# Kernel tuning notes

Measured on AMD Instinct MI355X. Metric: run time of the kernel, lower is better.

## Reference

```python
import jax, jax.numpy as jnp
import numpy as np

NUM_PRICAPS, DIM_PRICAPS = 1152, 8
NUM_OBJCAPS, DIM_OBJCAPS = 10, 16
ROUTINGS = 3


def squash(v, axis=-1):
    norm = jnp.linalg.norm(v, axis=axis, keepdims=True)
    scale = norm ** 2 / (1.0 + norm ** 2) / (norm + 1e-8)
    return scale * v


def conv2d(x, w, b, stride):
    out = jax.lax.conv_general_dilated(
        x, w, window_strides=(stride, stride), padding='VALID',
        dimension_numbers=('NCHW', 'OIHW', 'NCHW'))
    return out + b[None, :, None, None]


def setup_inputs() -> dict:
    key = jax.random.key(0)
    ks = jax.random.split(key, 12)
    f32 = jnp.float32
    x = jax.random.uniform(ks[0], (512, 1, 28, 28), dtype=f32)
    conv1_w = jax.random.normal(ks[1], (256, 1, 9, 9), f32) / np.sqrt(1 * 81)
    conv1_b = jnp.zeros((256,), f32)
    conv2_w = jax.random.normal(ks[2], (256, 256, 9, 9), f32) / np.sqrt(256 * 81)
    conv2_b = jnp.zeros((256,), f32)
    route_w = 0.1 * jax.random.normal(ks[3], (NUM_OBJCAPS, NUM_PRICAPS, DIM_OBJCAPS, DIM_PRICAPS), f32)
    d_in = NUM_OBJCAPS * DIM_OBJCAPS  # 160
    dec1_w = jax.random.normal(ks[4], (512, d_in), f32) / np.sqrt(d_in)
    dec1_b = jnp.zeros((512,), f32)
    dec2_w = jax.random.normal(ks[5], (1024, 512), f32) / np.sqrt(512)
    dec2_b = jnp.zeros((1024,), f32)
    dec3_w = jax.random.normal(ks[6], (784, 1024), f32) / np.sqrt(1024)
    dec3_b = jnp.zeros((784,), f32)
    return {'x': x, 'conv1_w': conv1_w, 'conv1_b': conv1_b,
            'conv2_w': conv2_w, 'conv2_b': conv2_b, 'route_w': route_w,
            'dec1_w': dec1_w, 'dec1_b': dec1_b, 'dec2_w': dec2_w,
            'dec2_b': dec2_b, 'dec3_w': dec3_w, 'dec3_b': dec3_b}


def reference(x, conv1_w, conv1_b, conv2_w, conv2_b, route_w,
              dec1_w, dec1_b, dec2_w, dec2_b, dec3_w, dec3_b):
    B = x.shape[0]
    # Encoder: two convs (no activation in original), then capsulate + squash
    h = conv2d(x, conv1_w, conv1_b, 1)            # [B,256,20,20]
    h = conv2d(h, conv2_w, conv2_b, 2)            # [B,256,6,6]
    pricaps = squash(jnp.transpose(h, (0, 2, 3, 1)).reshape(B, NUM_PRICAPS, DIM_PRICAPS))
    # Votes: weight [o,i,k,d] @ incaps [b,i,d] -> [b,o,i,k]
    hat = jnp.einsum('oikd,bid->boik', route_w, pricaps)  # [B,10,1152,16]
    hat_det = jax.lax.stop_gradient(hat)
    b_log = jnp.zeros((B, NUM_OBJCAPS, NUM_PRICAPS), x.dtype)
    c = jax.nn.softmax(jnp.ones((B, NUM_OBJCAPS, NUM_PRICAPS), x.dtype), axis=1)
    outcaps = None
    for i in range(ROUTINGS):
        if i < ROUTINGS - 1:
            outcaps = squash(jnp.sum(c[:, :, :, None] * hat_det, axis=2, keepdims=True))  # [B,10,1,16]
            b_log = b_log + jnp.sum(outcaps * hat_det, axis=-1)
            c = jax.nn.softmax(b_log, axis=1)
        else:
            outcaps = squash(jnp.sum(c[:, :, :, None] * hat, axis=2, keepdims=True))
    objcaps = outcaps[:, :, 0, :]                 # [B,10,16]
    objcaps_len = jnp.linalg.norm(objcaps, axis=-1)  # [B,10]
    # Decoder: reconstruct only the max-length class capsule
    idx_max = jnp.argmax(objcaps_len, axis=1)
    y_onehot = jax.nn.one_hot(idx_max, NUM_OBJCAPS, dtype=objcaps.dtype)
    oc = (objcaps * y_onehot[:, :, None]).reshape(B, -1)  # [B,160]
    d = jax.nn.relu(oc @ dec1_w.T + dec1_b)
    d = jax.nn.relu(d @ dec2_w.T + dec2_b)
    d = jax.nn.sigmoid(d @ dec3_w.T + dec3_b)
    x_recon = jnp.clip(d.reshape(B, 1, 28, 28), 0.0, 1.0)
    return (objcaps_len, x_recon)
```

## Files before the change

### kernel.cpp

```cpp
#include <hip/hip_runtime.h>

typedef short short8 __attribute__((ext_vector_type(8)));
typedef float floatx4 __attribute__((ext_vector_type(4)));

__device__ __forceinline__ unsigned short bf16rn(float x) {
  union { float f; unsigned int u; } v; v.f = x;
  unsigned int r = v.u + 0x7fffu + ((v.u >> 16) & 1u);
  return (unsigned short)(r >> 16);
}
__device__ __forceinline__ float bf16f(unsigned short h) {
  union { unsigned int u; float f; } v; v.u = ((unsigned int)h) << 16;
  return v.f;
}
__device__ __forceinline__ void gload16(const void* g, void* l) {
  __builtin_amdgcn_global_load_lds((const __attribute__((address_space(1))) unsigned int*)g,
                                   (__attribute__((address_space(3))) unsigned int*)l, 16, 0, 0);
}
__device__ __forceinline__ unsigned swz128(int row) {
  return ((row & 1) << 6) | ((row & 2) << 4) | ((row & 4) << 2);
}
__device__ __forceinline__ unsigned s4of(int row) {
  return ((row & 1) << 2) | (row & 2) | ((row & 4) >> 2);
}

__global__ __launch_bounds__(256) void k_w2p(const float* __restrict__ w2,
                                             unsigned short* __restrict__ w2p) {
  __shared__ float sm[20736];
  const int t = threadIdx.x;
  const int co = blockIdx.x;
  for (int q = t; q < 20736; q += 256) sm[q] = w2[(size_t)co * 20736 + q];
  __syncthreads();
  const unsigned s4 = s4of(co);
  unsigned short* base = w2p + (size_t)co * 64;
  for (int q = t; q < 5184; q += 256) {
    int kk = q >> 6, r = q & 63, cb = r >> 3, cp = r & 7;
    unsigned src = (unsigned)cp ^ s4;
    int half = src >> 2, oct = src & 3;
    const float* col = &sm[(cb * 32 + oct * 8) * 81 + kk];
    union { unsigned short u[8]; uint4 v; } pk;
#pragma unroll
    for (int j = 0; j < 8; ++j) {
      float v = col[j * 81];
      unsigned short hi = bf16rn(v);
      pk.u[j] = half ? bf16rn(v - bf16f(hi)) : hi;
    }
    *(uint4*)(base + (size_t)(kk * 8 + cb) * 16384 + cp * 8) = pk.v;
  }
}

__global__ __launch_bounds__(256) void k_conv1(const float* __restrict__ x, const float* __restrict__ w1,
                                               const float* __restrict__ b1,
                                               unsigned short* __restrict__ h1h,
                                               unsigned short* __restrict__ h1l, int b0) {
  __shared__ float xs[784];
  __shared__ float wsm[64 * 81];
  const int t = threadIdx.x;
  const int b = b0 + blockIdx.x;
  const int coq = blockIdx.y;
  for (int q = t; q < 784; q += 256) xs[q] = x[(size_t)b * 784 + q];
  for (int q = t; q < 5184; q += 256) wsm[q] = w1[coq * 5184 + q];
  __syncthreads();
  const int col = t & 63, yg = t >> 6;
  const int co = coq * 64 + col;
  const float bv = b1[co];
  unsigned short* oh = h1h + (size_t)blockIdx.x * 102400 + co;
  unsigned short* ol = h1l + (size_t)blockIdx.x * 102400 + co;
  for (int yy = 0; yy < 5; ++yy) {
    const int y = yg * 5 + yy;
    float acc[20];
#pragma unroll
    for (int i = 0; i < 20; ++i) acc[i] = bv;
    for (int ky = 0; ky < 9; ++ky) {
      float row[28];
#pragma unroll
      for (int cc = 0; cc < 28; ++cc) row[cc] = xs[(y + ky) * 28 + cc];
#pragma unroll
      for (int kx = 0; kx < 9; ++kx) {
        float wv = wsm[col * 81 + ky * 9 + kx];
#pragma unroll
        for (int xx = 0; xx < 20; ++xx) acc[xx] += row[xx + kx] * wv;
      }
    }
#pragma unroll
    for (int xx = 0; xx < 20; ++xx) {
      unsigned short hi = bf16rn(acc[xx]);
      unsigned short lo = bf16rn(acc[xx] - bf16f(hi));
      size_t p = (size_t)(y * 20 + xx) * 256;
      oh[p] = hi; ol[p] = lo;
    }
  }
}

__global__ __launch_bounds__(256) void k_conv2m(const unsigned short* __restrict__ h1h,
                                                const unsigned short* __restrict__ h1l,
                                                const unsigned short* __restrict__ w2p,
                                                float* __restrict__ part, int b0) {
  __shared__ __align__(16) char smem[40960];
  const int t = threadIdx.x;
  const int lin = blockIdx.x + 144 * blockIdx.z;
  const int xcd = lin & 7, idx = lin >> 3;
  const int zz = xcd & 3;
  const int n0 = ((xcd >> 2) * 72 + idx) * 64;
  const int kk0 = (zz == 0) ? 0 : (21 + 20 * (zz - 1));
  const int kkn = (zz == 0) ? 21 : 20;

  const int wid = t >> 6, lane = t & 63;
  const int l15 = lane & 15, l4 = lane >> 4;
  const int brow = t >> 2, bc4 = t & 3;
  size_t bsrc;
  {
    int nloc = n0 + brow;
    int bi = nloc / 36, pp = nloc - bi * 36;
    int oy = pp / 6, ox = pp - oy * 6;
    bsrc = ((size_t)((bi * 20 + 2 * oy) * 20 + 2 * ox)) * 256;
  }
  const unsigned bswz = swz128(brow);
  const unsigned bo_hi = (unsigned)(brow * 128) + (((unsigned)(bc4 * 16)) ^ bswz);
  const unsigned bo_lo = (unsigned)(brow * 128) + (((unsigned)(64 + bc4 * 16)) ^ bswz);

  floatx4 acc[4][4];
#pragma unroll
  for (int i = 0; i < 4; ++i)
#pragma unroll
    for (int j = 0; j < 4; ++j) acc[i][j] = (floatx4)0.f;

  for (int kq = 0; kq < kkn; ++kq) {
    const int kk = kk0 + kq;
    const int ky = kk / 9, kx = kk - ky * 9;
    const int koff = (ky * 20 + kx) * 256;
    for (int cb = 0; cb < 8; ++cb) {
      const unsigned short* abase = w2p + (size_t)(kk * 8 + cb) * 16384;
#pragma unroll
      for (int j = 0; j < 8; ++j) {
        const int seg = j * 4 + wid;
        gload16(abase + seg * 512 + lane * 8, smem + seg * 1024);
      }
      {
        const unsigned short* sh = h1h + bsrc + koff + cb * 32 + bc4 * 8;
        const unsigned short* sl = h1l + bsrc + koff + cb * 32 + bc4 * 8;
        uint4 vh = *(const uint4*)sh;
        uint4 vl = *(const uint4*)sl;
        *(uint4*)(smem + 32768 + bo_hi) = vh;
        *(uint4*)(smem + 32768 + bo_lo) = vl;
      }
      __syncthreads();
      short8 bh[4], blo[4];
#pragma unroll
      for (int nf = 0; nf < 4; ++nf) {
        const int br = nf * 16 + l15;
        const unsigned s = swz128(br);
        bh[nf] = *(const short8*)(smem + 32768 + br * 128 + (((unsigned)(l4 * 16)) ^ s));
        blo[nf] = *(const short8*)(smem + 32768 + br * 128 + (((unsigned)(64 + l4 * 16)) ^ s));
      }
#pragma unroll
      for (int mf = 0; mf < 4; ++mf) {
        const int ar = wid * 64 + mf * 16 + l15;
        const unsigned s = swz128(ar);
        short8 ah = *(const short8*)(smem + ar * 128 + (((unsigned)(l4 * 16)) ^ s));
        short8 al = *(const short8*)(smem + ar * 128 + (((unsigned)(64 + l4 * 16)) ^ s));
#pragma unroll
        for (int nf = 0; nf < 4; ++nf) {
          acc[mf][nf] = __builtin_amdgcn_mfma_f32_16x16x32_bf16(ah, bh[nf], acc[mf][nf], 0, 0, 0);
          acc[mf][nf] = __builtin_amdgcn_mfma_f32_16x16x32_bf16(ah, blo[nf], acc[mf][nf], 0, 0, 0);
          acc[mf][nf] = __builtin_amdgcn_mfma_f32_16x16x32_bf16(al, bh[nf], acc[mf][nf], 0, 0, 0);
        }
      }
      __syncthreads();
    }
  }
  float* po = part + (size_t)zz * 4718592;
#pragma unroll
  for (int mf = 0; mf < 4; ++mf) {
#pragma unroll
    for (int nf = 0; nf < 4; ++nf) {
      int cog = wid * 64 + mf * 16 + l4 * 4;
      int ng = b0 * 36 + n0 + nf * 16 + l15;
      *(floatx4*)&po[(size_t)ng * 256 + cog] = acc[mf][nf];
    }
  }
}

__global__ __launch_bounds__(256) void k_redsquash(const float* __restrict__ part,
                                                   const float* __restrict__ b2,
                                                   float* __restrict__ pri) {
  const int idx = blockIdx.x * 256 + threadIdx.x;
  const int n = idx >> 5, cap = idx & 31;
  const size_t o = (size_t)n * 256 + cap * 8;
  float s[8];
#pragma unroll
  for (int j = 0; j < 8; ++j) s[j] = b2[cap * 8 + j];
#pragma unroll
  for (int z = 0; z < 4; ++z) {
    const float4 a0 = *(const float4*)&part[(size_t)z * 4718592 + o];
    const float4 a1 = *(const float4*)&part[(size_t)z * 4718592 + o + 4];
    s[0] += a0.x; s[1] += a0.y; s[2] += a0.z; s[3] += a0.w;
    s[4] += a1.x; s[5] += a1.y; s[6] += a1.z; s[7] += a1.w;
  }
  float ss = 0.f;
#pragma unroll
  for (int j = 0; j < 8; ++j) ss += s[j] * s[j];
  float nn = sqrtf(ss);
  float sc = ss / (1.f + ss) / (nn + 1e-8f);
  float4 o0, o1;
  o0.x = s[0] * sc; o0.y = s[1] * sc; o0.z = s[2] * sc; o0.w = s[3] * sc;
  o1.x = s[4] * sc; o1.y = s[5] * sc; o1.z = s[6] * sc; o1.w = s[7] * sc;
  *(float4*)&pri[o] = o0;
  *(float4*)&pri[o + 4] = o1;
}

__global__ __launch_bounds__(256) void k_rwp(const float* __restrict__ rw,
                                             unsigned short* __restrict__ rwpa) {
  __shared__ float sm[8192];
  const int t = threadIdx.x;
  const int o = blockIdx.x / 18, ic = blockIdx.x % 18;
  const float* src = rw + (size_t)o * 147456 + (size_t)ic * 8192;
  for (int q = t; q < 8192; q += 256) sm[q] = src[q];
  __syncthreads();
  const int r = t;
  const int c32 = r >> 4, kobj = r & 15;
  const unsigned s4 = s4of(r);
  unsigned short* base = rwpa + (size_t)blockIdx.x * 16384 + r * 64;
#pragma unroll
  for (int cp = 0; cp < 8; ++cp) {
    unsigned c = (unsigned)cp ^ s4;
    int half = c >> 2;
    int il = c32 * 4 + (c & 3);
    const float* col = &sm[il * 128 + kobj * 8];
    union { unsigned short u[8]; uint4 v; } pk;
#pragma unroll
    for (int e = 0; e < 8; ++e) {
      float v = col[e];
      unsigned short hi = bf16rn(v);
      pk.u[e] = half ? bf16rn(v - bf16f(hi)) : hi;
    }
    *(uint4*)(base + cp * 8) = pk.v;
  }
}

__global__ __launch_bounds__(256, 2) void k_passA(const unsigned short* __restrict__ rwpa,
                                                  const float* __restrict__ pri,
                                                  const float* __restrict__ cbuf,
                                                  float* __restrict__ spart, int iter) {
  __shared__ __align__(16) char smem[65536];
  const int t = threadIdx.x;
  const int b0 = blockIdx.x * 16, ic = blockIdx.y, o = blockIdx.z;
  const int i0 = ic * 64;
  {
    const unsigned short* abase = rwpa + (size_t)(o * 18 + ic) * 16384;
    const int wid = t >> 6, lane = t & 63;
#pragma unroll
    for (int j = 0; j < 8; ++j) {
      const int seg = j * 4 + wid;
      gload16(abase + seg * 512 + lane * 8, smem + seg * 1024);
    }
  }
  const int bl = t >> 4, c32 = t & 15;
  {
    const float* psrc = pri + (size_t)(b0 + bl) * 9216 + i0 * 8 + c32 * 32;
    float pv[32];
#pragma unroll
    for (int j = 0; j < 8; ++j) {
      float4 v = *(const float4*)&psrc[j * 4];
      pv[j * 4 + 0] = v.x; pv[j * 4 + 1] = v.y; pv[j * 4 + 2] = v.z; pv[j * 4 + 3] = v.w;
    }
    float cv[4];
    if (iter == 0) {
      cv[0] = cv[1] = cv[2] = cv[3] = 0.1f;
    } else {
      float4 cc = *(const float4*)&cbuf[(size_t)((b0 + bl) * 10 + o) * 1152 + i0 + c32 * 4];
      cv[0] = cc.x; cv[1] = cc.y; cv[2] = cc.z; cv[3] = cc.w;
    }
    union { unsigned short u[32]; uint4 v[4]; } qh, ql;
#pragma unroll
    for (int m = 0; m < 32; ++m) {
      float q = cv[m >> 3] * pv[m];
      unsigned short hi = bf16rn(q);
      qh.u[m] = hi;
      ql.u[m] = bf16rn(q - bf16f(hi));
    }
    const int r = c32 * 16 + bl;
    const unsigned swz = swz128(r);
    char* qbase = smem + 32768 + r * 128;
#pragma unroll
    for (int j = 0; j < 8; ++j) {
      int c = (j + c32) & 7;
      uint4 v = (c < 4) ? qh.v[c & 3] : ql.v[c & 3];
      *(uint4*)(qbase + (((unsigned)(c * 16)) ^ swz)) = v;
    }
  }
  __syncthreads();
  const int wid = t >> 6, lane = t & 63;
  const int l15 = lane & 15, l4 = lane >> 4;
  floatx4 acc = (floatx4)0.f;
#pragma unroll
  for (int cc = 0; cc < 4; ++cc) {
    const int kc = wid * 4 + cc;
    const int rr = kc * 16 + l15;
    const unsigned s = swz128(rr);
    short8 ah  = *(const short8*)(smem + rr * 128 + (((unsigned)(l4 * 16)) ^ s));
    short8 al  = *(const short8*)(smem + rr * 128 + (((unsigned)(64 + l4 * 16)) ^ s));
    short8 bh  = *(const short8*)(smem + 32768 + rr * 128 + (((unsigned)(l4 * 16)) ^ s));
    short8 blo = *(const short8*)(smem + 32768 + rr * 128 + (((unsigned)(64 + l4 * 16)) ^ s));
    acc = __builtin_amdgcn_mfma_f32_16x16x32_bf16(ah, bh, acc, 0, 0, 0);
    acc = __builtin_amdgcn_mfma_f32_16x16x32_bf16(ah, blo, acc, 0, 0, 0);
    acc = __builtin_amdgcn_mfma_f32_16x16x32_bf16(al, bh, acc, 0, 0, 0);
  }
  __syncthreads();
  *(floatx4*)(smem + wid * 1024 + (l15 * 16 + l4 * 4) * 4) = acc;
  __syncthreads();
  {
    const int obl = t >> 4, okj = t & 15;
    const float* pp = (const float*)smem;
    float s = pp[obl * 16 + okj] + pp[256 + obl * 16 + okj] +
              pp[512 + obl * 16 + okj] + pp[768 + obl * 16 + okj];
    spart[((size_t)blockIdx.y * 512 + (b0 + obl)) * 160 + o * 16 + okj] = s;
  }
}

__global__ __launch_bounds__(256) void k_reduce(const float* __restrict__ spart, float* __restrict__ outc,
                                                float* __restrict__ len_out, int final_) {
  const int t = threadIdx.x;
  const int b = blockIdx.x;
  if (t >= 160) return;
  const int o = t / 16, d = t & 15;
  float s = 0.f;
  for (int ic = 0; ic < 18; ++ic) s += spart[((size_t)ic * 512 + b) * 160 + t];
  float ss = s * s;
  ss += __shfl_xor(ss, 1, 16);
  ss += __shfl_xor(ss, 2, 16);
  ss += __shfl_xor(ss, 4, 16);
  ss += __shfl_xor(ss, 8, 16);
  float n = sqrtf(ss);
  float sc = ss / (1.f + ss) / (n + 1e-8f);
  outc[(size_t)b * 160 + t] = sc * s;
  if (final_ && d == 0) len_out[b * 10 + o] = sc * n;
}

__global__ __launch_bounds__(256, 2) void k_passB(const float* __restrict__ rw, const float* __restrict__ pri,
                                                  const float* __restrict__ outc, float* __restrict__ blog,
                                                  int accum) {
  __shared__ __align__(16) float rw_s[16 * 516];
  __shared__ __align__(16) float p_s[16 * 516];
  __shared__ float oc_s[256];
  const int t = threadIdx.x;
  const int b0 = blockIdx.x * 16, i0 = blockIdx.y * 64, o = blockIdx.z;
  const float* rsrc = rw + (size_t)o * 147456 + (size_t)i0 * 128;
  for (int m = t; m < 2048; m += 256) {
    int il = m >> 5, r = m & 31, d = r >> 1, kh = (m & 1) * 4;
    float4 v = *(const float4*)&rsrc[il * 128 + d * 8 + kh];
    *(float4*)&rw_s[d * 516 + il * 8 + kh] = v;
  }
  for (int m = t; m < 2048; m += 256) {
    int bl = m >> 7, off = (m & 127) * 4;
    float4 v = *(const float4*)&pri[(size_t)(b0 + bl) * 9216 + i0 * 8 + off];
    *(float4*)&p_s[bl * 516 + off] = v;
  }
  oc_s[t] = outc[(size_t)(b0 + (t >> 4)) * 160 + o * 16 + (t & 15)];
  __syncthreads();
  const int il0 = t & 15, bl = t >> 4;
  float ocv[16];
#pragma unroll
  for (int k = 0; k < 16; ++k) ocv[k] = oc_s[bl * 16 + k];
#pragma unroll
  for (int is = 0; is < 4; ++is) {
    const int il = is * 16 + il0;
    float4 p0 = *(float4*)&p_s[bl * 516 + il * 8];
    float4 p1 = *(float4*)&p_s[bl * 516 + il * 8 + 4];
    float acc = 0.f;
#pragma unroll
    for (int dd = 0; dd < 16; ++dd) {
      float4 r0 = *(float4*)&rw_s[dd * 516 + il * 8];
      float4 r1 = *(float4*)&rw_s[dd * 516 + il * 8 + 4];
      float h = r0.x * p0.x + r0.y * p0.y + r0.z * p0.z + r0.w * p0.w +
                r1.x * p1.x + r1.y * p1.y + r1.z * p1.z + r1.w * p1.w;
      acc += h * ocv[dd];
    }
    size_t gi = (size_t)((b0 + bl) * 10 + o) * 1152 + i0 + il;
    blog[gi] = accum ? (blog[gi] + acc) : acc;
  }
}

__global__ __launch_bounds__(256) void k_softmax(const float* __restrict__ blog, float* __restrict__ cbuf) {
  const int b = blockIdx.x;
  const int i = blockIdx.y * 256 + threadIdx.x;
  if (i >= 1152) return;
  float v[10];
  float m = -1e30f;
#pragma unroll
  for (int o = 0; o < 10; ++o) {
    v[o] = blog[(size_t)(b * 10 + o) * 1152 + i];
    m = fmaxf(m, v[o]);
  }
  float s = 0.f;
#pragma unroll
  for (int o = 0; o < 10; ++o) {
    v[o] = __expf(v[o] - m);
    s += v[o];
  }
  float inv = 1.f / s;
#pragma unroll
  for (int o = 0; o < 10; ++o) cbuf[(size_t)(b * 10 + o) * 1152 + i] = v[o] * inv;
}

__global__ __launch_bounds__(256) void k_argmax(const float* __restrict__ len_, const float* __restrict__ outc,
                                                int* __restrict__ win, float* __restrict__ oc16) {
  const int b = blockIdx.x * 256 + threadIdx.x;
  if (b >= 512) return;
  float best = len_[b * 10];
  int wi = 0;
  for (int o = 1; o < 10; ++o) {
    float v = len_[b * 10 + o];
    if (v > best) { best = v; wi = o; }
  }
  win[b] = wi;
  for (int k = 0; k < 16; ++k) oc16[b * 16 + k] = outc[(size_t)b * 160 + wi * 16 + k];
}

__global__ __launch_bounds__(256) void k_dec1(const float* __restrict__ oc16, const int* __restrict__ win,
                                              const float* __restrict__ w, const float* __restrict__ bias,
                                              float* __restrict__ d1) {
  const int b = blockIdx.x, t = threadIdx.x;
  const int wi = win[b];
  float ocv[16];
#pragma unroll
  for (int k = 0; k < 16; ++k) ocv[k] = oc16[b * 16 + k];
#pragma unroll
  for (int rep = 0; rep < 2; ++rep) {
    int j = t + rep * 256;
    const float* wr = w + (size_t)j * 160 + wi * 16;
    float acc = bias[j];
#pragma unroll
    for (int k = 0; k < 16; ++k) acc += ocv[k] * wr[k];
    d1[(size_t)b * 512 + j] = fmaxf(acc, 0.f);
  }
}

template <int K, int ACT>
__global__ __launch_bounds__(256) void k_fc(const float* __restrict__ in, const float* __restrict__ w,
                                            const float* __restrict__ bias, float* __restrict__ out, int M) {
  __shared__ __align__(16) float w_s[16 * 64];
  __shared__ __align__(16) float i_s[16 * 64];
  const int t = threadIdx.x;
  const int j0 = blockIdx.x * 64, b0 = blockIdx.y * 64;
  const int tx = t & 15, ty = t >> 4;
  const int jl = tx * 4, bl = ty * 4;
  float acc[4][4];
#pragma unroll
  for (int i = 0; i < 4; ++i)
#pragma unroll
    for (int j = 0; j < 4; ++j) acc[i][j] = 0.f;
  const int rr = t >> 2, kq = (t & 3) * 4;
  for (int k0 = 0; k0 < K; k0 += 16) {
    __syncthreads();
    float4 wv = make_float4(0.f, 0.f, 0.f, 0.f);
    if (j0 + rr < M) wv = *(const float4*)&w[(size_t)(j0 + rr) * K + k0 + kq];
    float4 iv = *(const float4*)&in[(size_t)(b0 + rr) * K + k0 + kq];
    w_s[(kq + 0) * 64 + rr] = wv.x;
    w_s[(kq + 1) * 64 + rr] = wv.y;
    w_s[(kq + 2) * 64 + rr] = wv.z;
    w_s[(kq + 3) * 64 + rr] = wv.w;
    i_s[(kq + 0) * 64 + rr] = iv.x;
    i_s[(kq + 1) * 64 + rr] = iv.y;
    i_s[(kq + 2) * 64 + rr] = iv.z;
    i_s[(kq + 3) * 64 + rr] = iv.w;
    __syncthreads();
#pragma unroll
    for (int k = 0; k < 16; ++k) {
      float4 a = *(float4*)&w_s[k * 64 + jl];
      float4 v = *(float4*)&i_s[k * 64 + bl];
      float av[4] = {a.x, a.y, a.z, a.w};
      float vv[4] = {v.x, v.y, v.z, v.w};
#pragma unroll
      for (int jj = 0; jj < 4; ++jj)
#pragma unroll
        for (int bb = 0; bb < 4; ++bb) acc[jj][bb] += av[jj] * vv[bb];
    }
  }
#pragma unroll
  for (int jj = 0; jj < 4; ++jj) {
    int j = j0 + jl + jj;
    if (j >= M) continue;
    float bs = bias[j];
#pragma unroll
    for (int bb = 0; bb < 4; ++bb) {
      float v = acc[jj][bb] + bs;
      if (ACT == 0) {
        v = fmaxf(v, 0.f);
      } else {
        v = 1.f / (1.f + __expf(-v));
        v = fminf(fmaxf(v, 0.f), 1.f);
      }
      out[(size_t)(b0 + bl + bb) * M + j] = v;
    }
  }
}

extern "C" void kernel_launch(void* const* d_in, const int* in_sizes, int n_in,
                              void* d_out, int out_size, void* d_ws, size_t ws_size,
                              hipStream_t stream) {
  (void)in_sizes; (void)n_in; (void)out_size; (void)ws_size;
  const float* x   = (const float*)d_in[0];
  const float* w1  = (const float*)d_in[1];
  const float* b1  = (const float*)d_in[2];
  const float* w2  = (const float*)d_in[3];
  const float* b2  = (const float*)d_in[4];
  const float* rw  = (const float*)d_in[5];
  const float* d1w = (const float*)d_in[6];
  const float* d1b = (const float*)d_in[7];
  const float* d2w = (const float*)d_in[8];
  const float* d2b = (const float*)d_in[9];
  const float* d3w = (const float*)d_in[10];
  const float* d3b = (const float*)d_in[11];
  float* out = (float*)d_out;

  char* wsb = (char*)d_ws;
  size_t cur = 0;
  auto alloc = [&](size_t bytes) -> char* {
    char* p = wsb + cur;
    cur += (bytes + 255) & ~(size_t)255;
    return p;
  };
  unsigned short* W2P = (unsigned short*)alloc(21233664);
  float* PART = (float*)alloc(75497472);
  float* PRI  = (float*)alloc(18874368);
  float* OUTC = (float*)alloc(327680);
  float* OC   = (float*)alloc(32768);
  int*   WIN  = (int*)alloc(2048);
  float* D1   = (float*)alloc(1048576);
  float* D2   = (float*)alloc(2097152);
  unsigned short* H1H = (unsigned short*)alloc(52428800);
  unsigned short* H1L = (unsigned short*)alloc(52428800);
  float* C  = (float*)H1H;
  float* BL = (float*)((char*)H1H + 23592960);
  float* SP = (float*)((char*)H1H + 47185920);
  unsigned short* RWPA = (unsigned short*)PART;

  k_w2p<<<256, 256, 0, stream>>>(w2, W2P);
  for (int b0 = 0; b0 < 512; b0 += 256) {
    k_conv1<<<dim3(256, 4), 256, 0, stream>>>(x, w1, b1, H1H, H1L, b0);
    k_conv2m<<<dim3(144, 1, 4), 256, 0, stream>>>(H1H, H1L, W2P, PART, b0);
  }
  k_redsquash<<<2304, 256, 0, stream>>>(PART, b2, PRI);
  k_rwp<<<180, 256, 0, stream>>>(rw, RWPA);

  dim3 gAB(32, 18, 10);
  k_passA<<<gAB, 256, 0, stream>>>(RWPA, PRI, C, SP, 0);
  k_reduce<<<512, 256, 0, stream>>>(SP, OUTC, out, 0);
  k_passB<<<gAB, 256, 0, stream>>>(rw, PRI, OUTC, BL, 0);
  k_softmax<<<dim3(512, 5), 256, 0, stream>>>(BL, C);
  k_passA<<<gAB, 256, 0, stream>>>(RWPA, PRI, C, SP, 1);
  k_reduce<<<512, 256, 0, stream>>>(SP, OUTC, out, 0);
  k_passB<<<gAB, 256, 0, stream>>>(rw, PRI, OUTC, BL, 1);
  k_softmax<<<dim3(512, 5), 256, 0, stream>>>(BL, C);
  k_passA<<<gAB, 256, 0, stream>>>(RWPA, PRI, C, SP, 2);
  k_reduce<<<512, 256, 0, stream>>>(SP, OUTC, out, 1);

  k_argmax<<<2, 256, 0, stream>>>(out, OUTC, WIN, OC);
  k_dec1<<<512, 256, 0, stream>>>(OC, WIN, d1w, d1b, D1);
  k_fc<512, 0><<<dim3(16, 8), 256, 0, stream>>>(D1, d2w, d2b, D2, 1024);
  k_fc<1024, 1><<<dim3(13, 8), 256, 0, stream>>>(D2, d3w, d3b, out + 5120, 784);
}
```

Measured before the change: 1.414 ms.

## Fuse routing pass A with squash reduce by looping over input-capsule chunks

The routing vote-sum kernel now loops over all 18 input-capsule chunks inside one block, accumulating in MFMA registers, then applies squash and writes output capsules directly. This removes the separate partial-sum buffer and the reduce kernel launch. The grid shrinks from 5760 blocks to 320 and each block runs the chunks serially with full syncs and no load/compute overlap, which may reduce parallelism and latency hiding on the GPU. The k_rwp indexing was simplified to an equivalent linear offset.

```diff
diff --git a/kernel.cpp b/kernel.cpp
--- a/kernel.cpp
+++ b/kernel.cpp
@@ -212,8 +212,7 @@
                                              unsigned short* __restrict__ rwpa) {
   __shared__ float sm[8192];
   const int t = threadIdx.x;
-  const int o = blockIdx.x / 18, ic = blockIdx.x % 18;
-  const float* src = rw + (size_t)o * 147456 + (size_t)ic * 8192;
+  const float* src = rw + (size_t)blockIdx.x * 8192;
   for (int q = t; q < 8192; q += 256) sm[q] = src[q];
   __syncthreads();
   const int r = t;
@@ -237,94 +236,84 @@
   }
 }
 
-__global__ __launch_bounds__(256, 2) void k_passA(const unsigned short* __restrict__ rwpa,
-                                                  const float* __restrict__ pri,
-                                                  const float* __restrict__ cbuf,
-                                                  float* __restrict__ spart, int iter) {
+__global__ __launch_bounds__(256, 2) void k_passAf(const unsigned short* __restrict__ rwpa,
+                                                   const float* __restrict__ pri,
+                                                   const float* __restrict__ cbuf,
+                                                   float* __restrict__ outc,
+                                                   float* __restrict__ len_out,
+                                                   int iter, int final_) {
   __shared__ __align__(16) char smem[65536];
   const int t = threadIdx.x;
-  const int b0 = blockIdx.x * 16, ic = blockIdx.y, o = blockIdx.z;
-  const int i0 = ic * 64;
-  {
-    const unsigned short* abase = rwpa + (size_t)(o * 18 + ic) * 16384;
-    const int wid = t >> 6, lane = t & 63;
-#pragma unroll
-    for (int j = 0; j < 8; ++j) {
-      const int seg = j * 4 + wid;
-      gload16(abase + seg * 512 + lane * 8, smem + seg * 1024);
-    }
-  }
-  const int bl = t >> 4, c32 = t & 15;
-  {
-    const float* psrc = pri + (size_t)(b0 + bl) * 9216 + i0 * 8 + c32 * 32;
-    float pv[32];
-#pragma unroll
-    for (int j = 0; j < 8; ++j) {
-      float4 v = *(const float4*)&psrc[j * 4];
-      pv[j * 4 + 0] = v.x; pv[j * 4 + 1] = v.y; pv[j * 4 + 2] = v.z; pv[j * 4 + 3] = v.w;
-    }
-    float cv[4];
-    if (iter == 0) {
-      cv[0] = cv[1] = cv[2] = cv[3] = 0.1f;
-    } else {
-      float4 cc = *(const float4*)&cbuf[(size_t)((b0 + bl) * 10 + o) * 1152 + i0 + c32 * 4];
-      cv[0] = cc.x; cv[1] = cc.y; cv[2] = cc.z; cv[3] = cc.w;
-    }
-    union { unsigned short u[32]; uint4 v[4]; } qh, ql;
-#pragma unroll
-    for (int m = 0; m < 32; ++m) {
-      float q = cv[m >> 3] * pv[m];
-      unsigned short hi = bf16rn(q);
-      qh.u[m] = hi;
-      ql.u[m] = bf16rn(q - bf16f(hi));
-    }
-    const int r = c32 * 16 + bl;
-    const unsigned swz = swz128(r);
-    char* qbase = smem + 32768 + r * 128;
-#pragma unroll
-    for (int j = 0; j < 8; ++j) {
-      int c = (j + c32) & 7;
-      uint4 v = (c < 4) ? qh.v[c & 3] : ql.v[c & 3];
-      *(uint4*)(qbase + (((unsigned)(c * 16)) ^ swz)) = v;
-    }
-  }
-  __syncthreads();
+  const int b0 = blockIdx.x * 16, o = blockIdx.y;
   const int wid = t >> 6, lane = t & 63;
   const int l15 = lane & 15, l4 = lane >> 4;
+  const int bl = t >> 4, c32 = t & 15;
+
   floatx4 acc = (floatx4)0.f;
-#pragma unroll
-  for (int cc = 0; cc < 4; ++cc) {
-    const int kc = wid * 4 + cc;
-    const int rr = kc * 16 + l15;
-    const unsigned s = swz128(rr);
-    short8 ah  = *(const short8*)(smem + rr * 128 + (((unsigned)(l4 * 16)) ^ s));
-    short8 al  = *(const short8*)(smem + rr * 128 + (((unsigned)(64 + l4 * 16)) ^ s));
-    short8 bh  = *(const short8*)(smem + 32768 + rr * 128 + (((unsigned)(l4 * 16)) ^ s));
-    short8 blo = *(const short8*)(smem + 32768 + rr * 128 + (((unsigned)(64 + l4 * 16)) ^ s));
-    acc = __builtin_amdgcn_mfma_f32_16x16x32_bf16(ah, bh, acc, 0, 0, 0);
-    acc = __builtin_amdgcn_mfma_f32_16x16x32_bf16(ah, blo, acc, 0, 0, 0);
-    acc = __builtin_amdgcn_mfma_f32_16x16x32_bf16(al, bh, acc, 0, 0, 0);
-  }
-  __syncthreads();
+  for (int ic = 0; ic < 18; ++ic) {
+    const int i0 = ic * 64;
+    {
+      const unsigned short* abase = rwpa + (size_t)(o * 18 + ic) * 16384;
+#pragma unroll
+      for (int j = 0; j < 8; ++j) {
+        const int seg = j * 4 + wid;
+        gload16(abase + seg * 512 + lane * 8, smem + seg * 1024);
+      }
+    }
+    {
+      const float* psrc = pri + (size_t)(b0 + bl) * 9216 + i0 * 8 + c32 * 32;
+      float pv[32];
+#pragma unroll
+      for (int j = 0; j < 8; ++j) {
+        float4 v = *(const float4*)&psrc[j * 4];
+        pv[j * 4 + 0] = v.x; pv[j * 4 + 1] = v.y; pv[j * 4 + 2] = v.z; pv[j * 4 + 3] = v.w;
+      }
+      float cv[4];
+      if (iter == 0) {
+        cv[0] = cv[1] = cv[2] = cv[3] = 0.1f;
+      } else {
+        float4 cc = *(const float4*)&cbuf[(size_t)((b0 + bl) * 10 + o) * 1152 + i0 + c32 * 4];
+        cv[0] = cc.x; cv[1] = cc.y; cv[2] = cc.z; cv[3] = cc.w;
+      }
+      union { unsigned short u[32]; uint4 v[4]; } qh, ql;
+#pragma unroll
+      for (int m = 0; m < 32; ++m) {
+        float q = cv[m >> 3] * pv[m];
+        unsigned short hi = bf16rn(q);
+        qh.u[m] = hi;
+        ql.u[m] = bf16rn(q - bf16f(hi));
+      }
+      const int r = c32 * 16 + bl;
+      const unsigned swz = swz128(r);
+      char* qbase = smem + 32768 + r * 128;
+#pragma unroll
+      for (int j = 0; j < 8; ++j) {
+        int c = (j + c32) & 7;
+        uint4 v = (c < 4) ? qh.v[c & 3] : ql.v[c & 3];
+        *(uint4*)(qbase + (((unsigned)(c * 16)) ^ swz)) = v;
+      }
+    }
+    __syncthreads();
+#pragma unroll
+    for (int cc = 0; cc < 4; ++cc) {
+      const int kc = wid * 4 + cc;
+      const int rr = kc * 16 + l15;
+      const unsigned s = swz128(rr);
+      short8 ah  = *(const short8*)(smem + rr * 128 + (((unsigned)(l4 * 16)) ^ s));
+      short8 al  = *(const short8*)(smem + rr * 128 + (((unsigned)(64 + l4 * 16)) ^ s));
+      short8 bh  = *(const short8*)(smem + 32768 + rr * 128 + (((unsigned)(l4 * 16)) ^ s));
+      short8 blo = *(const short8*)(smem + 32768 + rr * 128 + (((unsigned)(64 + l4 * 16)) ^ s));
+      acc = __builtin_amdgcn_mfma_f32_16x16x32_bf16(ah, bh, acc, 0, 0, 0);
+      acc = __builtin_amdgcn_mfma_f32_16x16x32_bf16(ah, blo, acc, 0, 0, 0);
+      acc = __builtin_amdgcn_mfma_f32_16x16x32_bf16(al, bh, acc, 0, 0, 0);
+    }
+    __syncthreads();
+  }
   *(floatx4*)(smem + wid * 1024 + (l15 * 16 + l4 * 4) * 4) = acc;
   __syncthreads();
-  {
-    const int obl = t >> 4, okj = t & 15;
-    const float* pp = (const float*)smem;
-    float s = pp[obl * 16 + okj] + pp[256 + obl * 16 + okj] +
-              pp[512 + obl * 16 + okj] + pp[768 + obl * 16 + okj];
-    spart[((size_t)blockIdx.y * 512 + (b0 + obl)) * 160 + o * 16 + okj] = s;
-  }
-}
-
-__global__ __launch_bounds__(256) void k_reduce(const float* __restrict__ spart, float* __restrict__ outc,
-                                                float* __restrict__ len_out, int final_) {
-  const int t = threadIdx.x;
-  const int b = blockIdx.x;
-  if (t >= 160) return;
-  const int o = t / 16, d = t & 15;
-  float s = 0.f;
-  for (int ic = 0; ic < 18; ++ic) s += spart[((size_t)ic * 512 + b) * 160 + t];
+  const float* pp = (const float*)smem;
+  float s = pp[bl * 16 + c32] + pp[256 + bl * 16 + c32] +
+            pp[512 + bl * 16 + c32] + pp[768 + bl * 16 + c32];
   float ss = s * s;
   ss += __shfl_xor(ss, 1, 16);
   ss += __shfl_xor(ss, 2, 16);
@@ -332,8 +321,8 @@
   ss += __shfl_xor(ss, 8, 16);
   float n = sqrtf(ss);
   float sc = ss / (1.f + ss) / (n + 1e-8f);
-  outc[(size_t)b * 160 + t] = sc * s;
-  if (final_ && d == 0) len_out[b * 10 + o] = sc * n;
+  outc[(size_t)(b0 + bl) * 160 + o * 16 + c32] = sc * s;
+  if (final_ && c32 == 0) len_out[(b0 + bl) * 10 + o] = sc * n;
 }
 
 __global__ __launch_bounds__(256, 2) void k_passB(const float* __restrict__ rw, const float* __restrict__ pri,
@@ -532,7 +521,6 @@
   unsigned short* H1L = (unsigned short*)alloc(52428800);
   float* C  = (float*)H1H;
   float* BL = (float*)((char*)H1H + 23592960);
-  float* SP = (float*)((char*)H1H + 47185920);
   unsigned short* RWPA = (unsigned short*)PART;
 
   k_w2p<<<256, 256, 0, stream>>>(w2, W2P);
@@ -543,17 +531,15 @@
   k_redsquash<<<2304, 256, 0, stream>>>(PART, b2, PRI);
   k_rwp<<<180, 256, 0, stream>>>(rw, RWPA);
 
-  dim3 gAB(32, 18, 10);
-  k_passA<<<gAB, 256, 0, stream>>>(RWPA, PRI, C, SP, 0);
-  k_reduce<<<512, 256, 0, stream>>>(SP, OUTC, out, 0);
-  k_passB<<<gAB, 256, 0, stream>>>(rw, PRI, OUTC, BL, 0);
+  dim3 gA(32, 10);
+  dim3 gB(32, 18, 10);
+  k_passAf<<<gA, 256, 0, stream>>>(RWPA, PRI, C, OUTC, out, 0, 0);
+  k_passB<<<gB, 256, 0, stream>>>(rw, PRI, OUTC, BL, 0);
   k_softmax<<<dim3(512, 5), 256, 0, stream>>>(BL, C);
-  k_passA<<<gAB, 256, 0, stream>>>(RWPA, PRI, C, SP, 1);
-  k_reduce<<<512, 256, 0, stream>>>(SP, OUTC, out, 0);
-  k_passB<<<gAB, 256, 0, stream>>>(rw, PRI, OUTC, BL, 1);
+  k_passAf<<<gA, 256, 0, stream>>>(RWPA, PRI, C, OUTC, out, 1, 0);
+  k_passB<<<gB, 256, 0, stream>>>(rw, PRI, OUTC, BL, 1);
   k_softmax<<<dim3(512, 5), 256, 0, stream>>>(BL, C);
-  k_passA<<<gAB, 256, 0, stream>>>(RWPA, PRI, C, SP, 2);
-  k_reduce<<<512, 256, 0, stream>>>(SP, OUTC, out, 1);
+  k_passAf<<<gA, 256, 0, stream>>>(RWPA, PRI, C, OUTC, out, 2, 1);
 
   k_argmax<<<2, 256, 0, stream>>>(out, OUTC, WIN, OC);
   k_dec1<<<512, 256, 0, stream>>>(OC, WIN, d1w, d1b, D1);
```

Measured after the change: 1.534 ms. 1.08x slower.
